# Kernel tuning notes

Hardware: AMD Instinct MI355X
Metric: run time of the kernel (lower is better)

## Reference

```python
import jax, jax.numpy as jnp
import numpy as np

D_THRESH = 0.5  # forward default d=0.5


def setup_inputs() -> dict:
    key = jax.random.key(0)
    C, P, D = 10, 1000, 1024
    # scale so pairwise distances (~sqrt(2D)*scale) straddle the 0.5 threshold
    feats = jax.random.normal(key, (C * P, D), dtype=jnp.float32) * 0.011
    ids_per_cls = jnp.arange(C * P, dtype=jnp.int64).reshape(C, P)
    return {"feats": feats, "ids_per_cls": ids_per_cls, "budget": 2000}


def reference(feats, ids_per_cls, budget):
    C, P = ids_per_cls.shape
    per_cls_budget = budget // C  # budget = int(budget / len(ids_per_cls_train))
    X = feats[ids_per_cls.reshape(-1)]  # [C*P, D] class-blocked representatives
    # pairwise euclidean distances (torch.cdist p=2), computed via gram trick
    sq = jnp.sum(X * X, axis=-1)  # [C*P]
    d2 = sq[:, None] + sq[None, :] - 2.0 * (X @ X.T)  # [C*P, C*P]
    dist = jnp.sqrt(jnp.maximum(d2, 0.0))
    # only count neighbors from OTHER classes (the per-class loop pops class i)
    cls = jnp.repeat(jnp.arange(C), P)  # [C*P]
    other = cls[:, None] != cls[None, :]  # [C*P, C*P] bool
    counts = jnp.sum((dist < D_THRESH) & other, axis=-1)  # [C*P] int
    counts = counts.reshape(C, P)
    # ascending sort by count, keep the `per_cls_budget` most-separated nodes
    order = jnp.argsort(counts, axis=-1)  # [C, P]
    sel = order[:, :per_cls_budget]  # [C, budget//C]
    ids_selected = jnp.take_along_axis(ids_per_cls, sel, axis=1).reshape(-1)
    return ids_selected, counts
```

## Files before the change

kernel.cpp:

```cpp
#include <hip/hip_runtime.h>

#define N_TOT 10000
#define CLS_P 1000
#define NC 10
#define D 1024

#define TM 128
#define DELTA 1.35e-5f
#define INV_SCALE2 4.8828125e-4f
#define ESC_LOC 256
#define KCHUNKS (D / 32)
#define NTILE ((N_TOT + TM - 1) / TM)

typedef _Float16 f16x8 __attribute__((ext_vector_type(8)));
typedef float f32x4 __attribute__((ext_vector_type(4)));
typedef const __attribute__((address_space(1))) unsigned int* gptr_t;
typedef __attribute__((address_space(3))) unsigned int* lptr_t;

__global__ void zero_kernel(int* __restrict__ out, int n) {
    int i = blockIdx.x * blockDim.x + threadIdx.x;
    if (i < n) out[i] = 0;
}

__global__ void prep_kernel(const float* __restrict__ feats, const int* __restrict__ ids,
                            unsigned short* __restrict__ Xh,
                            double* __restrict__ sqd, float* __restrict__ sqf) {
    int row = blockIdx.x;
    int id = ids[row];
    const float4* rp = (const float4*)(feats + (size_t)id * D);
    float4 v = rp[threadIdx.x];
    float f[4] = {v.x, v.y, v.z, v.w};
    ushort4 hv;
    unsigned short* hp = &hv.x;
    double s = 0.0;
    #pragma unroll
    for (int e = 0; e < 4; e++) {
        s += (double)f[e] * f[e];
        union { _Float16 h; unsigned short u; } cv;
        cv.h = (_Float16)(f[e] * 64.0f);
        hp[e] = cv.u;
    }
    *(ushort4*)(Xh + (size_t)row * D + threadIdx.x * 4) = hv;

    #pragma unroll
    for (int off = 32; off > 0; off >>= 1)
        s += __shfl_down(s, off, 64);
    __shared__ double wsum[4];
    int lane = threadIdx.x & 63, wv = threadIdx.x >> 6;
    if (lane == 0) wsum[wv] = s;
    __syncthreads();
    if (threadIdx.x == 0) {
        double t = wsum[0] + wsum[1] + wsum[2] + wsum[3];
        sqd[row] = t;
        sqf[row] = (float)t;
    }
}

__launch_bounds__(256, 3)
__global__ void count_kernel(const unsigned short* __restrict__ Xh,
                             const float* __restrict__ sqf,
                             const double* __restrict__ sqd,
                             const float* __restrict__ feats,
                             const int* __restrict__ ids,
                             int* __restrict__ counts) {
    int bid = blockIdx.y * gridDim.x + blockIdx.x;
    int it_t = 0, jt_t = 0;
    {
        int rem = bid, band = 0;
        while (true) {
            int h = NTILE - band * 8; if (h > 8) h = 8;
            int area = h * NTILE;
            if (rem < area) { it_t = band * 8 + rem % h; jt_t = rem / h; break; }
            rem -= area; band++;
        }
    }
    const int ib = it_t * TM, jb = jt_t * TM;
    if (jb < ib) return;

    {
        int ci0 = ib / CLS_P, ci1 = (ib + TM - 1) / CLS_P;
        int cj0 = jb / CLS_P, cj1 = (jb + TM - 1) / CLS_P;
        if (ci0 == ci1 && cj0 == cj1 && ci0 == cj0) return;
    }

    __shared__ unsigned short S[3 * 8192];
    __shared__ int cred_i[TM], cred_j[TM];
    __shared__ int esc_n;
    __shared__ int2 esc_buf[ESC_LOC];

    const int tid = threadIdx.x;
    const int lane = tid & 63, w = tid >> 6;
    const int wi = (w & 1) * 64, wj = (w >> 1) * 64;
    const int quad = lane >> 4, col = lane & 15;

    if (tid == 0) esc_n = 0;

    const int warr = w >> 1;
    const int w01 = w & 1;
    const int rl0 = lane >> 2;
    const int slot = lane & 3;
    const int q = (slot - rl0 - (rl0 >> 2)) & 3;
    const int rowbase = warr ? jb : ib;

    const unsigned short* src[4];
    #pragma unroll
    for (int b = 0; b < 4; b++) {
        int grow = rowbase + b * 32 + w01 * 16 + rl0;
        if (grow > N_TOT - 1) grow = N_TOT - 1;
        src[b] = Xh + (size_t)grow * D + q * 8;
    }

#define STAGE(KC_, BUFBASE_)                                                     \
    {                                                                            \
        _Pragma("unroll")                                                        \
        for (int b = 0; b < 4; b++) {                                            \
            __builtin_amdgcn_global_load_lds(                                    \
                (gptr_t)(src[b] + (KC_) * 32),                                   \
                (lptr_t)((BUFBASE_) + warr * 4096 + b * 1024 + w01 * 512),       \
                16, 0, 0);                                                       \
        }                                                                        \
    }

#define FRAGS_(AH, BH, BUFBASE_)                                                 \
    {                                                                            \
        _Pragma("unroll")                                                        \
        for (int t = 0; t < 4; t++) {                                            \
            int rA = wi + t * 16 + col;                                          \
            int sA = (quad + rA + (rA >> 2)) & 3;                                \
            AH[t] = *(const f16x8*)((BUFBASE_) + rA * 32 + sA * 8);              \
            int rB = wj + t * 16 + col;                                          \
            int sB = (quad + rB + (rB >> 2)) & 3;                                \
            BH[t] = *(const f16x8*)((BUFBASE_) + 4096 + rB * 32 + sB * 8);       \
        }                                                                        \
    }

#define MFMA16_(AH, BH)                                                          \
    {                                                                            \
        _Pragma("unroll")                                                        \
        for (int it = 0; it < 4; it++)                                           \
            _Pragma("unroll")                                                    \
            for (int jt = 0; jt < 4; jt++)                                       \
                acc[it][jt] = __builtin_amdgcn_mfma_f32_16x16x32_f16(AH[it], BH[jt], acc[it][jt], 0, 0, 0); \
    }

#define WAIT4_BAR asm volatile("s_waitcnt vmcnt(4)\ns_barrier" ::: "memory")
#define WAIT0_BAR asm volatile("s_waitcnt vmcnt(0)\ns_barrier" ::: "memory")

    f32x4 acc[4][4];
    #pragma unroll
    for (int it = 0; it < 4; it++)
        #pragma unroll
        for (int jt = 0; jt < 4; jt++)
            acc[it][jt] = (f32x4){0.f, 0.f, 0.f, 0.f};

    f16x8 ah0[4], bh0[4], ah1[4], bh1[4];

    unsigned short* p0 = S;
    unsigned short* p1 = S + 8192;
    unsigned short* p2 = S + 16384;

    STAGE(0, p0);
    STAGE(1, p1);
    WAIT4_BAR;
    FRAGS_(ah0, bh0, p0);

    for (int kc = 0; kc < KCHUNKS - 2; kc += 2) {
        STAGE(kc + 2, p2);
        WAIT4_BAR;
        FRAGS_(ah1, bh1, p1);
        MFMA16_(ah0, bh0);
        { unsigned short* t = p0; p0 = p1; p1 = p2; p2 = t; }

        STAGE(kc + 3, p2);
        WAIT4_BAR;
        FRAGS_(ah0, bh0, p1);
        MFMA16_(ah1, bh1);
        { unsigned short* t = p0; p0 = p1; p1 = p2; p2 = t; }
    }
    WAIT0_BAR;
    FRAGS_(ah1, bh1, p1);
    MFMA16_(ah0, bh0);
    MFMA16_(ah1, bh1);

    if (tid < TM) { cred_i[tid] = 0; cred_j[tid] = 0; }
    __syncthreads();

    const float thr_lo = 0.25f - DELTA;
    const float thr_hi = 0.25f + DELTA;
    const bool diag = (ib == jb);

    float sqj[4];
    int clsj[4], jv[4], jidx[4];
    #pragma unroll
    for (int jt = 0; jt < 4; jt++) {
        int j = jb + wj + jt * 16 + col;
        jidx[jt] = j;
        jv[jt] = (j < N_TOT);
        sqj[jt] = jv[jt] ? sqf[j] : 0.f;
        clsj[jt] = j / CLS_P;
    }

    int cj[4] = {0, 0, 0, 0};

    #pragma unroll
    for (int it = 0; it < 4; it++) {
        #pragma unroll
        for (int r = 0; r < 4; r++) {
            int irow = wi + it * 16 + quad * 4 + r;
            int i = ib + irow;
            bool iv = (i < N_TOT);
            float sqi = iv ? sqf[i] : 0.f;
            int clsi = i / CLS_P;
            int ci = 0;
            #pragma unroll
            for (int jt = 0; jt < 4; jt++) {
                int j = jidx[jt];
                bool ok = iv && jv[jt] && (clsj[jt] != clsi) && (!diag || j > i);
                float d2 = sqi + sqj[jt] - acc[it][jt][r] * INV_SCALE2;
                bool in = ok && (d2 < thr_lo);
                bool esc = ok && !in && (d2 < thr_hi);
                ci += in ? 1 : 0;
                cj[jt] += in ? 1 : 0;
                if (esc) {
                    int k = atomicAdd(&esc_n, 1);
                    if (k < ESC_LOC) {
                        esc_buf[k] = make_int2(i, j);
                    } else {
                        const float* xi = feats + (size_t)ids[i] * D;
                        const float* xj = feats + (size_t)ids[j] * D;
                        double s = 0.0;
                        for (int kk = 0; kk < D; kk++) s += (double)xi[kk] * xj[kk];
                        if (sqd[i] + sqd[j] - 2.0 * s < 0.25) {
                            atomicAdd(&counts[i], 1);
                            atomicAdd(&counts[j], 1);
                        }
                    }
                }
            }
            ci += __shfl_xor(ci, 1, 64);
            ci += __shfl_xor(ci, 2, 64);
            ci += __shfl_xor(ci, 4, 64);
            ci += __shfl_xor(ci, 8, 64);
            if (col == 0 && ci) atomicAdd(&cred_i[irow], ci);
        }
    }
    #pragma unroll
    for (int jt = 0; jt < 4; jt++) {
        int v = cj[jt];
        v += __shfl_xor(v, 16, 64);
        v += __shfl_xor(v, 32, 64);
        if (quad == 0 && v) atomicAdd(&cred_j[wj + jt * 16 + col], v);
    }
    __syncthreads();
    if (tid < TM) {
        int i = ib + tid;
        if (i < N_TOT && cred_i[tid]) atomicAdd(&counts[i], cred_i[tid]);
        int j = jb + tid;
        if (j < N_TOT && cred_j[tid]) atomicAdd(&counts[j], cred_j[tid]);
    }
    __syncthreads();

    int n = esc_n; if (n > ESC_LOC) n = ESC_LOC;
    const int sub = lane >> 4, l16 = lane & 15;
    for (int p = w * 4 + sub; p < n; p += 16) {
        int2 pr = esc_buf[p];
        const float* xi = feats + (size_t)ids[pr.x] * D;
        const float* xj = feats + (size_t)ids[pr.y] * D;
        double s = 0.0;
        int k0 = l16 * 64;
        #pragma unroll
        for (int k = 0; k < 64; k += 4) {
            float4 a = *(const float4*)(xi + k0 + k);
            float4 b = *(const float4*)(xj + k0 + k);
            s += (double)a.x * b.x + (double)a.y * b.y + (double)a.z * b.z + (double)a.w * b.w;
        }
        s += __shfl_xor(s, 1, 64);
        s += __shfl_xor(s, 2, 64);
        s += __shfl_xor(s, 4, 64);
        s += __shfl_xor(s, 8, 64);
        if (l16 == 0) {
            double d2 = sqd[pr.x] + sqd[pr.y] - 2.0 * s;
            if (d2 < 0.25) {
                atomicAdd(&counts[pr.x], 1);
                atomicAdd(&counts[pr.y], 1);
            }
        }
    }
}

__global__ void sel_kernel(const int* __restrict__ counts, const int* __restrict__ ids,
                           int* __restrict__ out_ids, int pcb) {
    int c = blockIdx.x;
    __shared__ int lc[CLS_P];
    for (int p = threadIdx.x; p < CLS_P; p += blockDim.x)
        lc[p] = counts[c * CLS_P + p];
    __syncthreads();
    int p = threadIdx.x;
    if (p < CLS_P) {
        int cp = lc[p];
        int rank = 0;
        for (int qq = 0; qq < CLS_P; qq++) {
            int cq = lc[qq];
            rank += (cq < cp) || (cq == cp && qq < p);
        }
        if (rank < pcb)
            out_ids[c * pcb + rank] = ids[c * CLS_P + p];
    }
}

extern "C" void kernel_launch(void* const* d_in, const int* in_sizes, int n_in,
                              void* d_out, int out_size, void* d_ws, size_t ws_size,
                              hipStream_t stream) {
    const float* feats = (const float*)d_in[0];
    const int* ids = (const int*)d_in[1];
    int budget = out_size - N_TOT;
    int pcb = budget / NC;
    int* out = (int*)d_out;
    int* counts_out = out + NC * pcb;

    char* ws = (char*)d_ws;
    const size_t XH_OFF = 0;
    const size_t SQD_OFF = XH_OFF + (size_t)N_TOT * D * 2;
    const size_t SQF_OFF = SQD_OFF + (size_t)N_TOT * 8;

    unsigned short* Xh = (unsigned short*)(ws + XH_OFF);
    double* sqd = (double*)(ws + SQD_OFF);
    float* sqf = (float*)(ws + SQF_OFF);

    zero_kernel<<<(out_size + 255) / 256, 256, 0, stream>>>(out, out_size);
    prep_kernel<<<N_TOT, 256, 0, stream>>>(feats, ids, Xh, sqd, sqf);
    dim3 grid(NTILE, NTILE);
    count_kernel<<<grid, 256, 0, stream>>>(Xh, sqf, sqd, feats, ids, counts_out);
    sel_kernel<<<NC, 1024, 0, stream>>>(counts_out, ids, out, pcb);
}
```

Baseline: 336.2 us.

## Enlarge Gram tiles to 256 with 8-wave blocks and a 4-stage LDS pipeline

Tiles of the Gram-matrix count kernel grow from 128x128 to 256x256 and each block now has 512 threads (8 waves, each computing 128x64). Launch is a 1D triangular grid, so upper-triangle blocks are no longer launched only to exit early, and block IDs are remapped so consecutive tiles land on the same XCD. The K loop uses a 4-slot LDS ring with A/B staging interleaved between MFMA halves, and raises wave priority around the MFMA bursts. The aim is more data reuse per byte loaded and less launch waste, at the cost of higher register and LDS use per block and coarser load balance.

New measurement: 426.2 us. 1.27x slower.

```diff
diff --git a/kernel.cpp b/kernel.cpp
--- a/kernel.cpp
+++ b/kernel.cpp
@@ -5,12 +5,17 @@
 #define NC 10
 #define D 1024
 
-#define TM 128
+#define TM 256
+#define NT2 40
+#define NWG ((NT2 * (NT2 + 1)) / 2)
+#define KT 32
 #define DELTA 1.35e-5f
 #define INV_SCALE2 4.8828125e-4f
 #define ESC_LOC 256
-#define KCHUNKS (D / 32)
-#define NTILE ((N_TOT + TM - 1) / TM)
+
+#define BUF_S 16384
+#define B_OFF 8192
+#define HALF_S 4096
 
 typedef _Float16 f16x8 __attribute__((ext_vector_type(8)));
 typedef float f32x4 __attribute__((ext_vector_type(4)));
@@ -56,131 +61,120 @@
     }
 }
 
-__launch_bounds__(256, 3)
+__launch_bounds__(512, 2)
 __global__ void count_kernel(const unsigned short* __restrict__ Xh,
                              const float* __restrict__ sqf,
                              const double* __restrict__ sqd,
                              const float* __restrict__ feats,
                              const int* __restrict__ ids,
                              int* __restrict__ counts) {
-    int bid = blockIdx.y * gridDim.x + blockIdx.x;
-    int it_t = 0, jt_t = 0;
+    int bid = blockIdx.x;
     {
-        int rem = bid, band = 0;
-        while (true) {
-            int h = NTILE - band * 8; if (h > 8) h = 8;
-            int area = h * NTILE;
-            if (rem < area) { it_t = band * 8 + rem % h; jt_t = rem / h; break; }
-            rem -= area; band++;
-        }
-    }
-    const int ib = it_t * TM, jb = jt_t * TM;
-    if (jb < ib) return;
+        const int q = NWG >> 3, rr = NWG & 7;
+        int xcd = bid & 7, idx = bid >> 3;
+        bid = (xcd < rr ? xcd * (q + 1) : rr * (q + 1) + (xcd - rr) * q) + idx;
+    }
+    int it = 0, rem = bid;
+    while (rem >= NT2 - it) { rem -= NT2 - it; ++it; }
+    const int jt = it + rem;
+    const int ib = it * TM, jb = jt * TM;
 
     {
-        int ci0 = ib / CLS_P, ci1 = (ib + TM - 1) / CLS_P;
-        int cj0 = jb / CLS_P, cj1 = (jb + TM - 1) / CLS_P;
+        int i1 = ib + TM - 1; if (i1 > N_TOT - 1) i1 = N_TOT - 1;
+        int j1 = jb + TM - 1; if (j1 > N_TOT - 1) j1 = N_TOT - 1;
+        int ci0 = ib / CLS_P, ci1 = i1 / CLS_P;
+        int cj0 = jb / CLS_P, cj1 = j1 / CLS_P;
         if (ci0 == ci1 && cj0 == cj1 && ci0 == cj0) return;
     }
 
-    __shared__ unsigned short S[3 * 8192];
+    __shared__ unsigned short S[4 * BUF_S];
     __shared__ int cred_i[TM], cred_j[TM];
     __shared__ int esc_n;
     __shared__ int2 esc_buf[ESC_LOC];
 
     const int tid = threadIdx.x;
     const int lane = tid & 63, w = tid >> 6;
-    const int wi = (w & 1) * 64, wj = (w >> 1) * 64;
+    const int wr = w >> 2, wc = w & 3;
     const int quad = lane >> 4, col = lane & 15;
 
     if (tid == 0) esc_n = 0;
 
-    const int warr = w >> 1;
-    const int w01 = w & 1;
-    const int rl0 = lane >> 2;
-    const int slot = lane & 3;
-    const int q = (slot - rl0 - (rl0 >> 2)) & 3;
-    const int rowbase = warr ? jb : ib;
-
-    const unsigned short* src[4];
-    #pragma unroll
-    for (int b = 0; b < 4; b++) {
-        int grow = rowbase + b * 32 + w01 * 16 + rl0;
-        if (grow > N_TOT - 1) grow = N_TOT - 1;
-        src[b] = Xh + (size_t)grow * D + q * 8;
-    }
-
-#define STAGE(KC_, BUFBASE_)                                                     \
-    {                                                                            \
-        _Pragma("unroll")                                                        \
-        for (int b = 0; b < 4; b++) {                                            \
-            __builtin_amdgcn_global_load_lds(                                    \
-                (gptr_t)(src[b] + (KC_) * 32),                                   \
-                (lptr_t)((BUFBASE_) + warr * 4096 + b * 1024 + w01 * 512),       \
-                16, 0, 0);                                                       \
-        }                                                                        \
-    }
-
-#define FRAGS_(AH, BH, BUFBASE_)                                                 \
-    {                                                                            \
-        _Pragma("unroll")                                                        \
-        for (int t = 0; t < 4; t++) {                                            \
-            int rA = wi + t * 16 + col;                                          \
-            int sA = (quad + rA + (rA >> 2)) & 3;                                \
-            AH[t] = *(const f16x8*)((BUFBASE_) + rA * 32 + sA * 8);              \
-            int rB = wj + t * 16 + col;                                          \
-            int sB = (quad + rB + (rB >> 2)) & 3;                                \
-            BH[t] = *(const f16x8*)((BUFBASE_) + 4096 + rB * 32 + sB * 8);       \
-        }                                                                        \
-    }
-
-#define MFMA16_(AH, BH)                                                          \
-    {                                                                            \
-        _Pragma("unroll")                                                        \
-        for (int it = 0; it < 4; it++)                                           \
-            _Pragma("unroll")                                                    \
-            for (int jt = 0; jt < 4; jt++)                                       \
-                acc[it][jt] = __builtin_amdgcn_mfma_f32_16x16x32_f16(AH[it], BH[jt], acc[it][jt], 0, 0, 0); \
-    }
-
-#define WAIT4_BAR asm volatile("s_waitcnt vmcnt(4)\ns_barrier" ::: "memory")
-#define WAIT0_BAR asm volatile("s_waitcnt vmcnt(0)\ns_barrier" ::: "memory")
-
-    f32x4 acc[4][4];
-    #pragma unroll
-    for (int it = 0; it < 4; it++)
-        #pragma unroll
-        for (int jt = 0; jt < 4; jt++)
-            acc[it][jt] = (f32x4){0.f, 0.f, 0.f, 0.f};
-
-    f16x8 ah0[4], bh0[4], ah1[4], bh1[4];
-
-    unsigned short* p0 = S;
-    unsigned short* p1 = S + 8192;
-    unsigned short* p2 = S + 16384;
-
-    STAGE(0, p0);
-    STAGE(1, p1);
-    WAIT4_BAR;
-    FRAGS_(ah0, bh0, p0);
-
-    for (int kc = 0; kc < KCHUNKS - 2; kc += 2) {
-        STAGE(kc + 2, p2);
-        WAIT4_BAR;
-        FRAGS_(ah1, bh1, p1);
-        MFMA16_(ah0, bh0);
-        { unsigned short* t = p0; p0 = p1; p1 = p2; p2 = t; }
-
-        STAGE(kc + 3, p2);
-        WAIT4_BAR;
-        FRAGS_(ah0, bh0, p1);
-        MFMA16_(ah1, bh1);
-        { unsigned short* t = p0; p0 = p1; p1 = p2; p2 = t; }
-    }
-    WAIT0_BAR;
-    FRAGS_(ah1, bh1, p1);
-    MFMA16_(ah0, bh0);
-    MFMA16_(ah1, bh1);
+    const int srow = (w << 4) + (lane >> 2);
+    const int swz = (lane & 3) ^ ((lane >> 2) & 3);
+    int gA0 = ib + srow;         if (gA0 > N_TOT - 1) gA0 = N_TOT - 1;
+    int gA1 = ib + 128 + srow;   if (gA1 > N_TOT - 1) gA1 = N_TOT - 1;
+    int gB0 = jb + srow;         if (gB0 > N_TOT - 1) gB0 = N_TOT - 1;
+    int gB1 = jb + 128 + srow;   if (gB1 > N_TOT - 1) gB1 = N_TOT - 1;
+    const unsigned short* sA0 = Xh + (size_t)gA0 * D + swz * 8;
+    const unsigned short* sA1 = Xh + (size_t)gA1 * D + swz * 8;
+    const unsigned short* sB0 = Xh + (size_t)gB0 * D + swz * 8;
+    const unsigned short* sB1 = Xh + (size_t)gB1 * D + swz * 8;
+    const int wdst = w << 9;
+
+#define STG_A(SLOT_, KS_) do {                                                         \
+    __builtin_amdgcn_global_load_lds((gptr_t)(sA0 + (KS_)),                            \
+        (lptr_t)(S + (SLOT_) * BUF_S + wdst), 16, 0, 0);                               \
+    __builtin_amdgcn_global_load_lds((gptr_t)(sA1 + (KS_)),                            \
+        (lptr_t)(S + (SLOT_) * BUF_S + HALF_S + wdst), 16, 0, 0);                      \
+} while (0)
+#define STG_B(SLOT_, KS_) do {                                                         \
+    __builtin_amdgcn_global_load_lds((gptr_t)(sB0 + (KS_)),                            \
+        (lptr_t)(S + (SLOT_) * BUF_S + B_OFF + wdst), 16, 0, 0);                       \
+    __builtin_amdgcn_global_load_lds((gptr_t)(sB1 + (KS_)),                            \
+        (lptr_t)(S + (SLOT_) * BUF_S + B_OFF + HALF_S + wdst), 16, 0, 0);              \
+} while (0)
+
+    const int sl = (quad ^ (col & 3)) << 3;
+    const int aoff = (wr << 12) + (col << 5) + sl;
+    const int boff = B_OFF + (wc << 11) + (col << 5) + sl;
+
+    f32x4 acc[8][4];
+    #pragma unroll
+    for (int m = 0; m < 8; ++m)
+        #pragma unroll
+        for (int n = 0; n < 4; ++n)
+            acc[m][n] = (f32x4){0.f, 0.f, 0.f, 0.f};
+
+    f16x8 a[4], b[4];
+
+    STG_A(0, 0);  STG_B(0, 0);
+    STG_A(1, 32); STG_B(1, 32);
+    asm volatile("s_waitcnt vmcnt(4)\ns_barrier" ::: "memory");
+
+    #pragma unroll 4
+    for (int kt = 0; kt < KT; ++kt) {
+        const unsigned short* bufp = S + (kt & 3) * BUF_S;
+        const int s2 = (kt + 2) & 3;
+        const int ks = ((kt + 2) & (KT - 1)) << 5;
+
+        #pragma unroll
+        for (int m = 0; m < 4; ++m) a[m] = *(const f16x8*)(bufp + aoff + m * 512);
+        #pragma unroll
+        for (int n = 0; n < 4; ++n) b[n] = *(const f16x8*)(bufp + boff + n * 512);
+        STG_A(s2, ks);
+        asm volatile("s_barrier" ::: "memory");
+        __builtin_amdgcn_s_setprio(1);
+        #pragma unroll
+        for (int m = 0; m < 4; ++m)
+            #pragma unroll
+            for (int n = 0; n < 4; ++n)
+                acc[m][n] = __builtin_amdgcn_mfma_f32_16x16x32_f16(a[m], b[n], acc[m][n], 0, 0, 0);
+        __builtin_amdgcn_s_setprio(0);
+        asm volatile("s_barrier" ::: "memory");
+
+        #pragma unroll
+        for (int m = 0; m < 4; ++m) a[m] = *(const f16x8*)(bufp + aoff + 2048 + m * 512);
+        STG_B(s2, ks);
+        asm volatile("s_barrier" ::: "memory");
+        __builtin_amdgcn_s_setprio(1);
+        #pragma unroll
+        for (int m = 0; m < 4; ++m)
+            #pragma unroll
+            for (int n = 0; n < 4; ++n)
+                acc[4 + m][n] = __builtin_amdgcn_mfma_f32_16x16x32_f16(a[m], b[n], acc[4 + m][n], 0, 0, 0);
+        __builtin_amdgcn_s_setprio(0);
+        asm volatile("s_waitcnt vmcnt(4)\ns_barrier" ::: "memory");
+    }
 
     if (tid < TM) { cred_i[tid] = 0; cred_j[tid] = 0; }
     __syncthreads();
@@ -190,37 +184,37 @@
     const bool diag = (ib == jb);
 
     float sqj[4];
-    int clsj[4], jv[4], jidx[4];
-    #pragma unroll
-    for (int jt = 0; jt < 4; jt++) {
-        int j = jb + wj + jt * 16 + col;
-        jidx[jt] = j;
-        jv[jt] = (j < N_TOT);
-        sqj[jt] = jv[jt] ? sqf[j] : 0.f;
-        clsj[jt] = j / CLS_P;
+    int clsj[4], jidx[4], jv[4];
+    #pragma unroll
+    for (int n = 0; n < 4; ++n) {
+        int j = jb + (wc << 6) + n * 16 + col;
+        jidx[n] = j;
+        jv[n] = (j < N_TOT);
+        sqj[n] = jv[n] ? sqf[j] : 0.f;
+        clsj[n] = j / CLS_P;
     }
 
     int cj[4] = {0, 0, 0, 0};
 
     #pragma unroll
-    for (int it = 0; it < 4; it++) {
-        #pragma unroll
-        for (int r = 0; r < 4; r++) {
-            int irow = wi + it * 16 + quad * 4 + r;
+    for (int m = 0; m < 8; ++m) {
+        #pragma unroll
+        for (int r = 0; r < 4; ++r) {
+            int irow = (wr << 7) + m * 16 + quad * 4 + r;
             int i = ib + irow;
             bool iv = (i < N_TOT);
             float sqi = iv ? sqf[i] : 0.f;
             int clsi = i / CLS_P;
             int ci = 0;
             #pragma unroll
-            for (int jt = 0; jt < 4; jt++) {
-                int j = jidx[jt];
-                bool ok = iv && jv[jt] && (clsj[jt] != clsi) && (!diag || j > i);
-                float d2 = sqi + sqj[jt] - acc[it][jt][r] * INV_SCALE2;
+            for (int n = 0; n < 4; ++n) {
+                int j = jidx[n];
+                bool ok = iv && jv[n] && (clsj[n] != clsi) && (!diag || j > i);
+                float d2 = sqi + sqj[n] - acc[m][n][r] * INV_SCALE2;
                 bool in = ok && (d2 < thr_lo);
                 bool esc = ok && !in && (d2 < thr_hi);
                 ci += in ? 1 : 0;
-                cj[jt] += in ? 1 : 0;
+                cj[n] += in ? 1 : 0;
                 if (esc) {
                     int k = atomicAdd(&esc_n, 1);
                     if (k < ESC_LOC) {
@@ -245,11 +239,11 @@
         }
     }
     #pragma unroll
-    for (int jt = 0; jt < 4; jt++) {
-        int v = cj[jt];
+    for (int n = 0; n < 4; ++n) {
+        int v = cj[n];
         v += __shfl_xor(v, 16, 64);
         v += __shfl_xor(v, 32, 64);
-        if (quad == 0 && v) atomicAdd(&cred_j[wj + jt * 16 + col], v);
+        if (quad == 0 && v) atomicAdd(&cred_j[(wc << 6) + n * 16 + col], v);
     }
     __syncthreads();
     if (tid < TM) {
@@ -260,9 +254,9 @@
     }
     __syncthreads();
 
-    int n = esc_n; if (n > ESC_LOC) n = ESC_LOC;
+    int ne = esc_n; if (ne > ESC_LOC) ne = ESC_LOC;
     const int sub = lane >> 4, l16 = lane & 15;
-    for (int p = w * 4 + sub; p < n; p += 16) {
+    for (int p = w * 4 + sub; p < ne; p += 32) {
         int2 pr = esc_buf[p];
         const float* xi = feats + (size_t)ids[pr.x] * D;
         const float* xj = feats + (size_t)ids[pr.y] * D;
@@ -270,9 +264,9 @@
         int k0 = l16 * 64;
         #pragma unroll
         for (int k = 0; k < 64; k += 4) {
-            float4 a = *(const float4*)(xi + k0 + k);
-            float4 b = *(const float4*)(xj + k0 + k);
-            s += (double)a.x * b.x + (double)a.y * b.y + (double)a.z * b.z + (double)a.w * b.w;
+            float4 a4 = *(const float4*)(xi + k0 + k);
+            float4 b4 = *(const float4*)(xj + k0 + k);
+            s += (double)a4.x * b4.x + (double)a4.y * b4.y + (double)a4.z * b4.z + (double)a4.w * b4.w;
         }
         s += __shfl_xor(s, 1, 64);
         s += __shfl_xor(s, 2, 64);
@@ -329,7 +323,6 @@
 
     zero_kernel<<<(out_size + 255) / 256, 256, 0, stream>>>(out, out_size);
     prep_kernel<<<N_TOT, 256, 0, stream>>>(feats, ids, Xh, sqd, sqf);
-    dim3 grid(NTILE, NTILE);
-    count_kernel<<<grid, 256, 0, stream>>>(Xh, sqf, sqd, feats, ids, counts_out);
+    count_kernel<<<NWG, 512, 0, stream>>>(Xh, sqf, sqd, feats, ids, counts_out);
     sel_kernel<<<NC, 1024, 0, stream>>>(counts_out, ids, out, pcb);
 }
```
